# Performance work log

Measured on AMD Instinct MI355X. Metric: run time of the kernel, lower is better.

Reference implementation:

```python
import jax, jax.numpy as jnp
import numpy as np

M, A, E, H = 2048, 64, 128, 256
NUM_BOND_TYPES, NUM_ATOM_TYPES = 4, 118

def setup_inputs() -> dict:
    key = jax.random.key(0)
    ks = jax.random.split(key, 12)
    s = 0.02
    return {
        'node_rep': jax.random.normal(ks[0], (M, A, H), jnp.float32),
        'edge_index': jax.random.randint(ks[1], (M, 2, E), 0, A, jnp.int32),
        'bond_type_target': jax.random.randint(ks[2], (M, E), 0, NUM_BOND_TYPES, jnp.int32),
        'atom_type_target': jax.random.randint(ks[3], (M, A), 0, NUM_ATOM_TYPES, jnp.int32),
        'Wp1': jax.random.normal(ks[4], (H, H), jnp.float32) * s, 'bp1': jnp.zeros((H,), jnp.float32),
        'Wp2': jax.random.normal(ks[5], (H, H), jnp.float32) * s, 'bp2': jnp.zeros((H,), jnp.float32),
        'Wb1': jax.random.normal(ks[6], (2 * H, H), jnp.float32) * s, 'bb1': jnp.zeros((H,), jnp.float32),
        'Wb2': jax.random.normal(ks[7], (H, NUM_BOND_TYPES), jnp.float32) * s, 'bb2': jnp.zeros((NUM_BOND_TYPES,), jnp.float32),
        'Wa1': jax.random.normal(ks[8], (H, H), jnp.float32) * s, 'ba1': jnp.zeros((H,), jnp.float32),
        'Wa2': jax.random.normal(ks[9], (H, NUM_ATOM_TYPES), jnp.float32) * s, 'ba2': jnp.zeros((NUM_ATOM_TYPES,), jnp.float32),
    }

def _mlp(x, W1, b1, W2, b2):
    return jnp.maximum(x @ W1 + b1, 0.0) @ W2 + b2

def reference(node_rep, edge_index, bond_type_target, atom_type_target,
              Wp1, bp1, Wp2, bp2, Wb1, bb1, Wb2, bb2, Wa1, ba1, Wa2, ba2):
    # bond_if_proj: per-atom 2-layer MLP (dropout=0 -> identity)  [M,A,H]
    proj = _mlp(node_rep, Wp1, bp1, Wp2, bp2)
    # gather bond endpoint reps: index_select over atoms per molecule  [M,E,H]
    start = jnp.take_along_axis(proj, edge_index[:, 0, :, None], axis=1)
    end = jnp.take_along_axis(proj, edge_index[:, 1, :, None], axis=1)
    bt_in = jnp.concatenate([start, end], axis=-1)            # [M,E,2H]
    bt_logits = _mlp(bt_in, Wb1, bb1, Wb2, bb2)               # [M,E,4]
    bt_logp = jax.nn.log_softmax(bt_logits, axis=-1)
    # per-molecule mean CE averaged over molecules == global mean (equal sizes)
    bond_type_loss = -jnp.mean(jnp.take_along_axis(bt_logp, bond_type_target[..., None], axis=-1))
    bond_type_acc = jnp.mean((jnp.argmax(bt_logits, axis=-1) == bond_type_target).astype(jnp.float32))
    # atom type classifier on raw node reps  [M,A,118]
    at_logits = _mlp(node_rep, Wa1, ba1, Wa2, ba2)
    at_logp = jax.nn.log_softmax(at_logits, axis=-1)
    atom_type_loss = -jnp.mean(jnp.take_along_axis(at_logp, atom_type_target[..., None], axis=-1))
    atom_type_acc = jnp.mean((jnp.argmax(at_logits, axis=-1) == atom_type_target).astype(jnp.float32))
    loss = 0.5 * bond_type_loss + 0.5 * atom_type_loss
    return loss, bond_type_acc, atom_type_acc
```

## Files before the change

kernel.cpp:

```cpp
#include <hip/hip_runtime.h>
#include <hip/hip_bf16.h>

typedef __bf16 bf16x8 __attribute__((ext_vector_type(8)));
typedef float f32x16 __attribute__((ext_vector_type(16)));

__device__ inline unsigned short f2bf(float f) {
  __hip_bfloat16 h = __float2bfloat16(f);
  return *reinterpret_cast<unsigned short*>(&h);
}
__device__ inline unsigned pack2bf(float a, float b) {
  return (unsigned)f2bf(a) | ((unsigned)f2bf(b) << 16);
}
__device__ inline uint2 pack4bf(float a, float b, float c, float d) {
  uint2 r; r.x = pack2bf(a, b); r.y = pack2bf(c, d); return r;
}
__device__ inline bf16x8 as_bf16x8(uint4 v) { return __builtin_bit_cast(bf16x8, v); }
__device__ inline float bitf(unsigned u) { return __builtin_bit_cast(float, u); }
__device__ inline f32x16 mfma16(bf16x8 a, bf16x8 b, f32x16 c) {
  return __builtin_amdgcn_mfma_f32_32x32x16_bf16(a, b, c, 0, 0, 0);
}

#define BROW(XB, KK)                                                           \
  ((XB) + ((((rw + l31) << 9) + ((KK) << 5) + (h << 4)) ^ swz))

#define GEMM8(XB, W1PTR, W2PTR)                                                \
  {                                                                            \
    const unsigned char* w1_ = (const unsigned char*)(W1PTR) +                 \
                               ((cw + l31) << 5) + (h << 4);                   \
    const unsigned char* w2_ = (const unsigned char*)(W2PTR) +                 \
                               ((cw + l31) << 5) + (h << 4);                   \
    u0 = zero; u1 = zero; v0 = zero; v1 = zero;                                \
    bf16x8 pB = *(const bf16x8*)BROW(XB, 0);                                   \
    uint4 pA0 = *(const uint4*)(w1_);                                          \
    uint4 pA1 = *(const uint4*)(w1_ + 1024);                                   \
    uint4 pC0 = *(const uint4*)(w2_);                                          \
    uint4 pC1 = *(const uint4*)(w2_ + 1024);                                   \
    _Pragma("clang loop unroll(disable)")                                      \
    for (int kk = 0; kk < 16; kk += 2) {                                       \
      bf16x8 qB = *(const bf16x8*)BROW(XB, kk + 1);                            \
      uint4 qA0 = *(const uint4*)(w1_ + ((kk + 1) << 13));                     \
      uint4 qA1 = *(const uint4*)(w1_ + ((kk + 1) << 13) + 1024);              \
      uint4 qC0 = *(const uint4*)(w2_ + ((kk + 1) << 13));                     \
      uint4 qC1 = *(const uint4*)(w2_ + ((kk + 1) << 13) + 1024);              \
      u0 = mfma16(as_bf16x8(pA0), pB, u0);                                     \
      u1 = mfma16(as_bf16x8(pA1), pB, u1);                                     \
      v0 = mfma16(as_bf16x8(pC0), pB, v0);                                     \
      v1 = mfma16(as_bf16x8(pC1), pB, v1);                                     \
      if (kk + 2 < 16) {                                                       \
        pB = *(const bf16x8*)BROW(XB, kk + 2);                                 \
        pA0 = *(const uint4*)(w1_ + ((kk + 2) << 13));                         \
        pA1 = *(const uint4*)(w1_ + ((kk + 2) << 13) + 1024);                  \
        pC0 = *(const uint4*)(w2_ + ((kk + 2) << 13));                         \
        pC1 = *(const uint4*)(w2_ + ((kk + 2) << 13) + 1024);                  \
      }                                                                        \
      u0 = mfma16(as_bf16x8(qA0), qB, u0);                                     \
      u1 = mfma16(as_bf16x8(qA1), qB, u1);                                     \
      v0 = mfma16(as_bf16x8(qC0), qB, v0);                                     \
      v1 = mfma16(as_bf16x8(qC1), qB, v1);                                     \
    }                                                                          \
  }

#define WB8(DB, ACC, C, BIASPTR)                                               \
  _Pragma("unroll")                                                            \
  for (int g = 0; g < 4; ++g) {                                                \
    int xr_ = rw + l31;                                                        \
    int col = cw + (C) * 32 + g * 8 + h * 4;                                   \
    float4 bb = *(const float4*)((BIASPTR) + col);                             \
    float v0_ = fmaxf(ACC[4 * g + 0] + bb.x, 0.f);                             \
    float v1_ = fmaxf(ACC[4 * g + 1] + bb.y, 0.f);                             \
    float v2_ = fmaxf(ACC[4 * g + 2] + bb.z, 0.f);                             \
    float v3_ = fmaxf(ACC[4 * g + 3] + bb.w, 0.f);                             \
    int off = ((xr_ << 9) + (col << 1)) ^ ((xr_ & 7) << 4);                    \
    *(uint2*)((DB) + off) = pack4bf(v0_, v1_, v2_, v3_);                       \
  }

#define WB8R(DB, ACC, C)                                                       \
  _Pragma("unroll")                                                            \
  for (int g = 0; g < 4; ++g) {                                                \
    int xr_ = rw + l31;                                                        \
    int col = cw + (C) * 32 + g * 8 + h * 4;                                   \
    int off = ((xr_ << 9) + (col << 1)) ^ ((xr_ & 7) << 4);                    \
    *(uint2*)((DB) + off) = pack4bf(ACC[4 * g + 0], ACC[4 * g + 1],            \
                                    ACC[4 * g + 2], ACC[4 * g + 3]);           \
  }

#define STAGE_X(DST, SRC)                                                      \
  _Pragma("unroll")                                                            \
  for (int it = 0; it < 4; ++it) {                                             \
    int lb = (it * 1024 + tid) * 16;                                           \
    int d_ = lb ^ (((lb >> 9) & 7) << 4);                                      \
    const float4* s4 = (const float4*)((SRC) + (lb >> 1));                     \
    float4 f0 = s4[0], f1 = s4[1];                                             \
    uint4 v_ = { pack2bf(f0.x, f0.y), pack2bf(f0.z, f0.w),                     \
                 pack2bf(f1.x, f1.y), pack2bf(f1.z, f1.w) };                   \
    *(uint4*)((DST) + d_) = v_;                                                \
  }

__global__ __launch_bounds__(256) void k_pack(
    const float* __restrict__ wp1, const float* __restrict__ wa1,
    const float* __restrict__ wa2,
    unsigned short* __restrict__ dp1, unsigned short* __restrict__ da1,
    unsigned short* __restrict__ da2, float* __restrict__ accum)
{
  int b = blockIdx.x, tid = threadIdx.x;
  if (b == 0 && tid < 8) accum[tid] = 0.f;
  const float* src; unsigned short* dst; int e, logN, Nreal;
  if (b < 256)       { src = wp1; dst = dp1; e = b * 256 + tid;          logN = 8; Nreal = 256; }
  else if (b < 512)  { src = wa1; dst = da1; e = (b - 256) * 256 + tid;  logN = 8; Nreal = 256; }
  else               { src = wa2; dst = da2; e = (b - 512) * 256 + tid;  logN = 7; Nreal = 118; }
  int dk = e & 15;
  int rest = e >> 4;
  int n = rest & ((1 << logN) - 1);
  int kk = rest >> logN;
  int k = kk * 16 + dk;
  float v = (n < Nreal) ? src[k * Nreal + n] : 0.f;
  dst[e] = f2bf(v);
}

__global__ __launch_bounds__(256) void k_fold(
    const float* __restrict__ wp2, const float* __restrict__ wb1,
    const float* __restrict__ bp2, const float* __restrict__ bb1,
    unsigned short* __restrict__ dct, unsigned short* __restrict__ dcb,
    float* __restrict__ bias_e)
{
  int b = blockIdx.x, n = threadIdx.x;
  if (b < 512) {
    int k = b & 255;
    int off = (b < 256) ? 0 : 256;
    float s = 0.f;
    for (int t = 0; t < 256; ++t)
      s += wp2[k * 256 + t] * wb1[(t + off) * 256 + n];
    unsigned short* dst = (b < 256) ? dct : dcb;
    dst[((k >> 4) * 256 + n) * 16 + (k & 15)] = f2bf(s);
  } else {
    float s = bb1[n];
    for (int t = 0; t < 256; ++t)
      s += bp2[t] * (wb1[t * 256 + n] + wb1[(256 + t) * 256 + n]);
    bias_e[n] = s;
  }
}

__global__ __launch_bounds__(1024, 4) void k_mol(
    const float* __restrict__ node, const int* __restrict__ eidx,
    const int* __restrict__ btt, const int* __restrict__ att,
    const unsigned short* __restrict__ wp1p, const float* __restrict__ bp1,
    const unsigned short* __restrict__ wctp, const unsigned short* __restrict__ wcbp,
    const float* __restrict__ bias_e, const float* __restrict__ wb2,
    const float* __restrict__ bb2,
    const unsigned short* __restrict__ wa1p, const float* __restrict__ ba1,
    const unsigned short* __restrict__ wa2p, const float* __restrict__ ba2,
    float* __restrict__ accum)
{
  __shared__ __align__(16) unsigned char bufA[65536];
  __shared__ __align__(16) unsigned char bufB[65536];
  __shared__ float s_bias[256];
  __shared__ float4 s_wb2[256];
  __shared__ float s_b2a[128];
  __shared__ float s_red[32];
  const int tid = threadIdx.x;
  const int lane = tid & 63;
  const int w = tid >> 6;
  const int l31 = lane & 31;
  const int h = lane >> 5;
  const int swz = (l31 & 7) << 4;
  const int rw = (w >> 2) * 32;
  const int cw = (w & 3) * 64;
  const int m = blockIdx.x;

  STAGE_X(bufA, node + (long)m * 32768);
  if (tid < 256) {
    s_bias[tid] = bias_e[tid];
    s_wb2[tid] = ((const float4*)wb2)[tid];
  }
  if (tid < 128) s_b2a[tid] = (tid < 118) ? ba2[tid] : 0.f;
  const int t_at = att[m * 128 + (tid >> 3)];
  __syncthreads();

  f32x16 zero = {};
  f32x16 u0, u1, v0, v1;

  GEMM8(bufA, wa1p, wp1p);
  WB8(bufB, u0, 0, ba1);
  WB8(bufB, u1, 1, ba1);
  __syncthreads();
  WB8(bufA, v0, 0, bp1);
  WB8(bufA, v1, 1, bp1);
  __syncthreads();

  f32x16 aL = zero;
  {
    const int cw2 = (w & 3) * 32;
    const unsigned char* wb_ = (const unsigned char*)wa2p +
                               ((cw2 + l31) << 5) + (h << 4);
    bf16x8 pB = *(const bf16x8*)BROW(bufB, 0);
    uint4 pA = *(const uint4*)(wb_);
    _Pragma("clang loop unroll(disable)")
    for (int kk = 0; kk < 16; kk += 2) {
      bf16x8 qB = *(const bf16x8*)BROW(bufB, kk + 1);
      uint4 qA = *(const uint4*)(wb_ + ((kk + 1) << 12));
      aL = mfma16(as_bf16x8(pA), pB, aL);
      if (kk + 2 < 16) {
        pB = *(const bf16x8*)BROW(bufB, kk + 2);
        pA = *(const uint4*)(wb_ + ((kk + 2) << 12));
      }
      aL = mfma16(as_bf16x8(qA), qB, aL);
    }
  }
  __syncthreads();

  {
    const int cw2 = (w & 3) * 32;
    const int r0 = rw + l31;
    const int rx = (r0 & 7) << 4;
    #pragma unroll
    for (int g = 0; g < 4; ++g) {
      int colb = cw2 + 8 * g + 4 * h;
      uint4 val;
      val.x = __builtin_bit_cast(unsigned, aL[4 * g + 0] + s_b2a[colb + 0]);
      val.y = __builtin_bit_cast(unsigned, aL[4 * g + 1] + s_b2a[colb + 1]);
      val.z = __builtin_bit_cast(unsigned, aL[4 * g + 2] + s_b2a[colb + 2]);
      val.w = __builtin_bit_cast(unsigned, aL[4 * g + 3] + s_b2a[colb + 3]);
      *(uint4*)(bufB + (((r0 << 9) + (colb << 2)) ^ rx)) = val;
    }
  }
  __syncthreads();

  {
    const int row = tid >> 3, g8 = tid & 7;
    const unsigned char* lr = bufB + (row << 9);
    const int rx = (row & 7) << 4;
    float mx = -3.0e38f; int am = 127;
    #pragma unroll
    for (int j = 0; j < 4; ++j) {
      int ch = g8 + 8 * j;
      if (ch < 30) {
        float4 f = *(const float4*)(lr + (((ch << 4)) ^ rx));
        int c = ch * 4;
        if (f.x > mx) { mx = f.x; am = c; }
        if (f.y > mx) { mx = f.y; am = c + 1; }
        if (c + 2 < 118 && f.z > mx) { mx = f.z; am = c + 2; }
        if (c + 3 < 118 && f.w > mx) { mx = f.w; am = c + 3; }
      }
    }
    #pragma unroll
    for (int d = 1; d < 8; d <<= 1) {
      float mo = __shfl_xor(mx, d); int amo = __shfl_xor(am, d);
      if (mo > mx || (mo == mx && amo < am)) { mx = mo; am = amo; }
    }
    float s = 0.f, vt = 0.f;
    #pragma unroll
    for (int j = 0; j < 4; ++j) {
      int ch = g8 + 8 * j;
      if (ch < 30) {
        float4 f = *(const float4*)(lr + (((ch << 4)) ^ rx));
        int c = ch * 4;
        s += __expf(f.x - mx);
        s += __expf(f.y - mx);
        if (c + 2 < 118) s += __expf(f.z - mx);
        if (c + 3 < 118) s += __expf(f.w - mx);
        if (c == t_at) vt = f.x;
        if (c + 1 == t_at) vt = f.y;
        if (c + 2 == t_at) vt = f.z;
        if (c + 3 == t_at) vt = f.w;
      }
    }
    #pragma unroll
    for (int d = 1; d < 8; d <<= 1) { s += __shfl_xor(s, d); vt += __shfl_xor(vt, d); }
    float ce = 0.f, cc = 0.f;
    if (g8 == 0) { ce = __logf(s) + mx - vt; cc = (am == t_at) ? 1.f : 0.f; }
    #pragma unroll
    for (int d = 1; d < 64; d <<= 1) { ce += __shfl_xor(ce, d); cc += __shfl_xor(cc, d); }
    if (lane == 0) { s_red[w * 2] = ce; s_red[w * 2 + 1] = cc; }
  }

  GEMM8(bufA, wctp, wcbp);
  const int e_ = tid >> 2;
  const int gmol = e_ >> 7;
  const int ee = e_ & 127;
  const int es = gmol * 64 + eidx[(2 * m + gmol) * 256 + ee];
  const int ed = gmol * 64 + eidx[(2 * m + gmol) * 256 + 128 + ee];
  const int etg = btt[(2 * m + gmol) * 128 + ee];
  const float b20 = bb2[0], b21 = bb2[1], b22 = bb2[2], b23 = bb2[3];
  __syncthreads();
  if (tid == 0) {
    float sa = 0.f, sb = 0.f;
    #pragma unroll
    for (int i = 0; i < 16; ++i) { sa += s_red[2 * i]; sb += s_red[2 * i + 1]; }
    atomicAdd(accum + 2, sa);
    atomicAdd(accum + 3, sb);
  }
  WB8R(bufA, u0, 0);
  WB8R(bufA, u1, 1);
  WB8R(bufB, v0, 0);
  WB8R(bufB, v1, 1);
  __syncthreads();

  {
    const int qf = tid & 3;
    float lg0 = 0.f, lg1 = 0.f, lg2 = 0.f, lg3 = 0.f;
    #pragma unroll
    for (int j = 0; j < 8; ++j) {
      int c0 = qf * 64 + j * 8;
      int offS = ((es << 9) + (c0 << 1)) ^ ((es & 7) << 4);
      int offD = ((ed << 9) + (c0 << 1)) ^ ((ed & 7) << 4);
      uint4 us = *(const uint4*)(bufA + offS);
      uint4 ud = *(const uint4*)(bufB + offD);
      const unsigned* pu = (const unsigned*)&us;
      const unsigned* pv = (const unsigned*)&ud;
      #pragma unroll
      for (int q = 0; q < 4; ++q) {
        unsigned ua = pu[q], ub = pv[q];
        int c = c0 + 2 * q;
        float hlo = bitf(ua << 16) + bitf(ub << 16) + s_bias[c];
        float hhi = bitf(ua & 0xffff0000u) + bitf(ub & 0xffff0000u) + s_bias[c + 1];
        hlo = fmaxf(hlo, 0.f); hhi = fmaxf(hhi, 0.f);
        float4 w0 = s_wb2[c], w1 = s_wb2[c + 1];
        lg0 = fmaf(hlo, w0.x, fmaf(hhi, w1.x, lg0));
        lg1 = fmaf(hlo, w0.y, fmaf(hhi, w1.y, lg1));
        lg2 = fmaf(hlo, w0.z, fmaf(hhi, w1.z, lg2));
        lg3 = fmaf(hlo, w0.w, fmaf(hhi, w1.w, lg3));
      }
    }
    lg0 += __shfl_xor(lg0, 1); lg1 += __shfl_xor(lg1, 1);
    lg2 += __shfl_xor(lg2, 1); lg3 += __shfl_xor(lg3, 1);
    lg0 += __shfl_xor(lg0, 2); lg1 += __shfl_xor(lg1, 2);
    lg2 += __shfl_xor(lg2, 2); lg3 += __shfl_xor(lg3, 2);
    float ce = 0.f, cc = 0.f;
    if (qf == 0) {
      float l0 = lg0 + b20, l1 = lg1 + b21, l2 = lg2 + b22, l3 = lg3 + b23;
      int t = etg;
      int am = 0; float mx = l0;
      if (l1 > mx) { mx = l1; am = 1; }
      if (l2 > mx) { mx = l2; am = 2; }
      if (l3 > mx) { mx = l3; am = 3; }
      float s = __expf(l0 - mx) + __expf(l1 - mx) + __expf(l2 - mx) + __expf(l3 - mx);
      float lt = (t == 0) ? l0 : (t == 1) ? l1 : (t == 2) ? l2 : l3;
      ce = __logf(s) + mx - lt;
      cc = (am == t) ? 1.f : 0.f;
    }
    #pragma unroll
    for (int d = 1; d < 64; d <<= 1) { ce += __shfl_xor(ce, d); cc += __shfl_xor(cc, d); }
    if (lane == 0) { s_red[w * 2] = ce; s_red[w * 2 + 1] = cc; }
    __syncthreads();
    if (tid == 0) {
      float sa = 0.f, sb = 0.f;
      #pragma unroll
      for (int i = 0; i < 16; ++i) { sa += s_red[2 * i]; sb += s_red[2 * i + 1]; }
      atomicAdd(accum + 0, sa);
      atomicAdd(accum + 1, sb);
    }
  }
}

__global__ __launch_bounds__(64) void k_final(const float* __restrict__ accum,
                                              float* __restrict__ out)
{
  if (threadIdx.x == 0) {
    float bce = accum[0] / 262144.f;
    float bcc = accum[1] / 262144.f;
    float ace = accum[2] / 131072.f;
    float acc_ = accum[3] / 131072.f;
    out[0] = 0.5f * bce + 0.5f * ace;
    out[1] = bcc;
    out[2] = acc_;
  }
}

extern "C" void kernel_launch(void* const* d_in, const int* in_sizes, int n_in,
                              void* d_out, int out_size, void* d_ws, size_t ws_size,
                              hipStream_t stream)
{
  const float* node = (const float*)d_in[0];
  const int* eidx   = (const int*)d_in[1];
  const int* btt    = (const int*)d_in[2];
  const int* att    = (const int*)d_in[3];
  const float* Wp1 = (const float*)d_in[4];
  const float* bp1 = (const float*)d_in[5];
  const float* Wp2 = (const float*)d_in[6];
  const float* bp2 = (const float*)d_in[7];
  const float* Wb1 = (const float*)d_in[8];
  const float* bb1 = (const float*)d_in[9];
  const float* Wb2 = (const float*)d_in[10];
  const float* bb2 = (const float*)d_in[11];
  const float* Wa1 = (const float*)d_in[12];
  const float* ba1 = (const float*)d_in[13];
  const float* Wa2 = (const float*)d_in[14];
  const float* ba2 = (const float*)d_in[15];

  char* ws = (char*)d_ws;
  float* accum = (float*)ws;
  unsigned short* dp1 = (unsigned short*)(ws + 256);
  unsigned short* da1 = (unsigned short*)(ws + 131328);
  unsigned short* da2 = (unsigned short*)(ws + 262400);
  unsigned short* dct = (unsigned short*)(ws + 327936);
  unsigned short* dcb = (unsigned short*)(ws + 459008);
  float* bias_e       = (float*)(ws + 590080);

  k_pack<<<640, 256, 0, stream>>>(Wp1, Wa1, Wa2, dp1, da1, da2, accum);
  k_fold<<<513, 256, 0, stream>>>(Wp2, Wb1, bp2, bb1, dct, dcb, bias_e);
  k_mol<<<1024, 1024, 0, stream>>>(node, eidx, btt, att, dp1, bp1, dct, dcb,
                                   bias_e, Wb2, bb2, da1, ba1, da2, ba2, accum);
  k_final<<<1, 64, 0, stream>>>(accum, (float*)d_out);
}
```

Measured before the change: 197.1 us.

## Process one molecule per 512-thread block with 2x2 register-tiled MFMA per wave

```diff
diff --git a/kernel.cpp b/kernel.cpp
--- a/kernel.cpp
+++ b/kernel.cpp
@@ -20,50 +20,45 @@
   return __builtin_amdgcn_mfma_f32_32x32x16_bf16(a, b, c, 0, 0, 0);
 }
 
-#define BROW(XB, KK)                                                           \
-  ((XB) + ((((rw + l31) << 9) + ((KK) << 5) + (h << 4)) ^ swz))
-
-#define GEMM8(XB, W1PTR, W2PTR)                                                \
+#define BR(XB, R, KK)                                                          \
+  ((XB) + (((((R) * 32 + l31) << 9) + ((KK) << 5) + (h << 4)) ^ swz))
+
+#define GEMMS(XB, WPTR)                                                        \
   {                                                                            \
-    const unsigned char* w1_ = (const unsigned char*)(W1PTR) +                 \
+    const unsigned char* wb_ = (const unsigned char*)(WPTR) +                  \
                                ((cw + l31) << 5) + (h << 4);                   \
-    const unsigned char* w2_ = (const unsigned char*)(W2PTR) +                 \
-                               ((cw + l31) << 5) + (h << 4);                   \
-    u0 = zero; u1 = zero; v0 = zero; v1 = zero;                                \
-    bf16x8 pB = *(const bf16x8*)BROW(XB, 0);                                   \
-    uint4 pA0 = *(const uint4*)(w1_);                                          \
-    uint4 pA1 = *(const uint4*)(w1_ + 1024);                                   \
-    uint4 pC0 = *(const uint4*)(w2_);                                          \
-    uint4 pC1 = *(const uint4*)(w2_ + 1024);                                   \
+    acc00 = zero; acc01 = zero; acc10 = zero; acc11 = zero;                    \
+    bf16x8 pB0 = *(const bf16x8*)BR(XB, 0, 0);                                 \
+    bf16x8 pB1 = *(const bf16x8*)BR(XB, 1, 0);                                 \
+    uint4 pA0 = *(const uint4*)(wb_);                                          \
+    uint4 pA1 = *(const uint4*)(wb_ + 1024);                                   \
     _Pragma("clang loop unroll(disable)")                                      \
     for (int kk = 0; kk < 16; kk += 2) {                                       \
-      bf16x8 qB = *(const bf16x8*)BROW(XB, kk + 1);                            \
-      uint4 qA0 = *(const uint4*)(w1_ + ((kk + 1) << 13));                     \
-      uint4 qA1 = *(const uint4*)(w1_ + ((kk + 1) << 13) + 1024);              \
-      uint4 qC0 = *(const uint4*)(w2_ + ((kk + 1) << 13));                     \
-      uint4 qC1 = *(const uint4*)(w2_ + ((kk + 1) << 13) + 1024);              \
-      u0 = mfma16(as_bf16x8(pA0), pB, u0);                                     \
-      u1 = mfma16(as_bf16x8(pA1), pB, u1);                                     \
-      v0 = mfma16(as_bf16x8(pC0), pB, v0);                                     \
-      v1 = mfma16(as_bf16x8(pC1), pB, v1);                                     \
+      bf16x8 qB0 = *(const bf16x8*)BR(XB, 0, kk + 1);                          \
+      bf16x8 qB1 = *(const bf16x8*)BR(XB, 1, kk + 1);                          \
+      uint4 qA0 = *(const uint4*)(wb_ + ((kk + 1) << 13));                     \
+      uint4 qA1 = *(const uint4*)(wb_ + ((kk + 1) << 13) + 1024);              \
+      acc00 = mfma16(as_bf16x8(pA0), pB0, acc00);                              \
+      acc10 = mfma16(as_bf16x8(pA1), pB0, acc10);                              \
+      acc01 = mfma16(as_bf16x8(pA0), pB1, acc01);                              \
+      acc11 = mfma16(as_bf16x8(pA1), pB1, acc11);                              \
       if (kk + 2 < 16) {                                                       \
-        pB = *(const bf16x8*)BROW(XB, kk + 2);                                 \
-        pA0 = *(const uint4*)(w1_ + ((kk + 2) << 13));                         \
-        pA1 = *(const uint4*)(w1_ + ((kk + 2) << 13) + 1024);                  \
-        pC0 = *(const uint4*)(w2_ + ((kk + 2) << 13));                         \
-        pC1 = *(const uint4*)(w2_ + ((kk + 2) << 13) + 1024);                  \
+        pB0 = *(const bf16x8*)BR(XB, 0, kk + 2);                               \
+        pB1 = *(const bf16x8*)BR(XB, 1, kk + 2);                               \
+        pA0 = *(const uint4*)(wb_ + ((kk + 2) << 13));                         \
+        pA1 = *(const uint4*)(wb_ + ((kk + 2) << 13) + 1024);                  \
       }                                                                        \
-      u0 = mfma16(as_bf16x8(qA0), qB, u0);                                     \
-      u1 = mfma16(as_bf16x8(qA1), qB, u1);                                     \
-      v0 = mfma16(as_bf16x8(qC0), qB, v0);                                     \
-      v1 = mfma16(as_bf16x8(qC1), qB, v1);                                     \
+      acc00 = mfma16(as_bf16x8(qA0), qB0, acc00);                              \
+      acc10 = mfma16(as_bf16x8(qA1), qB0, acc10);                              \
+      acc01 = mfma16(as_bf16x8(qA0), qB1, acc01);                              \
+      acc11 = mfma16(as_bf16x8(qA1), qB1, acc11);                              \
     }                                                                          \
   }
 
-#define WB8(DB, ACC, C, BIASPTR)                                               \
+#define WB22(DB, ACC, R, C, BIASPTR)                                           \
   _Pragma("unroll")                                                            \
   for (int g = 0; g < 4; ++g) {                                                \
-    int xr_ = rw + l31;                                                        \
+    int xr_ = (R) * 32 + l31;                                                  \
     int col = cw + (C) * 32 + g * 8 + h * 4;                                   \
     float4 bb = *(const float4*)((BIASPTR) + col);                             \
     float v0_ = fmaxf(ACC[4 * g + 0] + bb.x, 0.f);                             \
@@ -74,10 +69,10 @@
     *(uint2*)((DB) + off) = pack4bf(v0_, v1_, v2_, v3_);                       \
   }
 
-#define WB8R(DB, ACC, C)                                                       \
+#define WB22R(DB, ACC, R, C)                                                   \
   _Pragma("unroll")                                                            \
   for (int g = 0; g < 4; ++g) {                                                \
-    int xr_ = rw + l31;                                                        \
+    int xr_ = (R) * 32 + l31;                                                  \
     int col = cw + (C) * 32 + g * 8 + h * 4;                                   \
     int off = ((xr_ << 9) + (col << 1)) ^ ((xr_ & 7) << 4);                    \
     *(uint2*)((DB) + off) = pack4bf(ACC[4 * g + 0], ACC[4 * g + 1],            \
@@ -87,7 +82,7 @@
 #define STAGE_X(DST, SRC)                                                      \
   _Pragma("unroll")                                                            \
   for (int it = 0; it < 4; ++it) {                                             \
-    int lb = (it * 1024 + tid) * 16;                                           \
+    int lb = (it * 512 + tid) * 16;                                            \
     int d_ = lb ^ (((lb >> 9) & 7) << 4);                                      \
     const float4* s4 = (const float4*)((SRC) + (lb >> 1));                     \
     float4 f0 = s4[0], f1 = s4[1];                                             \
@@ -140,7 +135,7 @@
   }
 }
 
-__global__ __launch_bounds__(1024, 4) void k_mol(
+__global__ __launch_bounds__(512, 4) void k_mol(
     const float* __restrict__ node, const int* __restrict__ eidx,
     const int* __restrict__ btt, const int* __restrict__ att,
     const unsigned short* __restrict__ wp1p, const float* __restrict__ bp1,
@@ -151,56 +146,65 @@
     const unsigned short* __restrict__ wa2p, const float* __restrict__ ba2,
     float* __restrict__ accum)
 {
-  __shared__ __align__(16) unsigned char bufA[65536];
-  __shared__ __align__(16) unsigned char bufB[65536];
+  __shared__ __align__(16) unsigned char bufA[32768];
+  __shared__ __align__(16) unsigned char bufB[32768];
   __shared__ float s_bias[256];
   __shared__ float4 s_wb2[256];
   __shared__ float s_b2a[128];
-  __shared__ float s_red[32];
+  __shared__ float s_red[16];
   const int tid = threadIdx.x;
   const int lane = tid & 63;
   const int w = tid >> 6;
   const int l31 = lane & 31;
   const int h = lane >> 5;
   const int swz = (l31 & 7) << 4;
-  const int rw = (w >> 2) * 32;
+  const int mat = w >> 2;
   const int cw = (w & 3) * 64;
   const int m = blockIdx.x;
 
-  STAGE_X(bufA, node + (long)m * 32768);
+  STAGE_X(bufA, node + (long)m * 16384);
   if (tid < 256) {
     s_bias[tid] = bias_e[tid];
     s_wb2[tid] = ((const float4*)wb2)[tid];
   }
   if (tid < 128) s_b2a[tid] = (tid < 118) ? ba2[tid] : 0.f;
-  const int t_at = att[m * 128 + (tid >> 3)];
+  const int t_at = att[m * 64 + (tid >> 3)];
   __syncthreads();
 
   f32x16 zero = {};
-  f32x16 u0, u1, v0, v1;
-
-  GEMM8(bufA, wa1p, wp1p);
-  WB8(bufB, u0, 0, ba1);
-  WB8(bufB, u1, 1, ba1);
-  __syncthreads();
-  WB8(bufA, v0, 0, bp1);
-  WB8(bufA, v1, 1, bp1);
+  f32x16 acc00, acc01, acc10, acc11;
+
+  GEMMS(bufA, mat ? wp1p : wa1p);
+  if (mat == 0) {
+    WB22(bufB, acc00, 0, 0, ba1);
+    WB22(bufB, acc10, 0, 1, ba1);
+    WB22(bufB, acc01, 1, 0, ba1);
+    WB22(bufB, acc11, 1, 1, ba1);
+  }
+  __syncthreads();
+  if (mat == 1) {
+    WB22(bufA, acc00, 0, 0, bp1);
+    WB22(bufA, acc10, 0, 1, bp1);
+    WB22(bufA, acc01, 1, 0, bp1);
+    WB22(bufA, acc11, 1, 1, bp1);
+  }
   __syncthreads();
 
   f32x16 aL = zero;
   {
     const int cw2 = (w & 3) * 32;
+    const int R2 = w >> 2;
     const unsigned char* wb_ = (const unsigned char*)wa2p +
                                ((cw2 + l31) << 5) + (h << 4);
-    bf16x8 pB = *(const bf16x8*)BROW(bufB, 0);
+    bf16x8 pB = *(const bf16x8*)BR(bufB, R2, 0);
     uint4 pA = *(const uint4*)(wb_);
     _Pragma("clang loop unroll(disable)")
     for (int kk = 0; kk < 16; kk += 2) {
-      bf16x8 qB = *(const bf16x8*)BROW(bufB, kk + 1);
+      bf16x8 qB = *(const bf16x8*)BR(bufB, R2, kk + 1);
       uint4 qA = *(const uint4*)(wb_ + ((kk + 1) << 12));
       aL = mfma16(as_bf16x8(pA), pB, aL);
       if (kk + 2 < 16) {
-        pB = *(const bf16x8*)BROW(bufB, kk + 2);
+        pB = *(const bf16x8*)BR(bufB, R2, kk + 2);
         pA = *(const uint4*)(wb_ + ((kk + 2) << 12));
       }
       aL = mfma16(as_bf16x8(qA), qB, aL);
@@ -210,7 +214,7 @@
 
   {
     const int cw2 = (w & 3) * 32;
-    const int r0 = rw + l31;
+    const int r0 = (w >> 2) * 32 + l31;
     const int rx = (r0 & 7) << 4;
     #pragma unroll
     for (int g = 0; g < 4; ++g) {
@@ -273,26 +277,30 @@
     if (lane == 0) { s_red[w * 2] = ce; s_red[w * 2 + 1] = cc; }
   }
 
-  GEMM8(bufA, wctp, wcbp);
-  const int e_ = tid >> 2;
-  const int gmol = e_ >> 7;
-  const int ee = e_ & 127;
-  const int es = gmol * 64 + eidx[(2 * m + gmol) * 256 + ee];
-  const int ed = gmol * 64 + eidx[(2 * m + gmol) * 256 + 128 + ee];
-  const int etg = btt[(2 * m + gmol) * 128 + ee];
+  GEMMS(bufA, mat ? wcbp : wctp);
+  const int es = eidx[m * 256 + (tid >> 2)];
+  const int ed = eidx[m * 256 + 128 + (tid >> 2)];
+  const int etg = btt[m * 128 + (tid >> 2)];
   const float b20 = bb2[0], b21 = bb2[1], b22 = bb2[2], b23 = bb2[3];
   __syncthreads();
   if (tid == 0) {
     float sa = 0.f, sb = 0.f;
     #pragma unroll
-    for (int i = 0; i < 16; ++i) { sa += s_red[2 * i]; sb += s_red[2 * i + 1]; }
+    for (int i = 0; i < 8; ++i) { sa += s_red[2 * i]; sb += s_red[2 * i + 1]; }
     atomicAdd(accum + 2, sa);
     atomicAdd(accum + 3, sb);
   }
-  WB8R(bufA, u0, 0);
-  WB8R(bufA, u1, 1);
-  WB8R(bufB, v0, 0);
-  WB8R(bufB, v1, 1);
+  if (mat == 0) {
+    WB22R(bufA, acc00, 0, 0);
+    WB22R(bufA, acc10, 0, 1);
+    WB22R(bufA, acc01, 1, 0);
+    WB22R(bufA, acc11, 1, 1);
+  } else {
+    WB22R(bufB, acc00, 0, 0);
+    WB22R(bufB, acc10, 0, 1);
+    WB22R(bufB, acc01, 1, 0);
+    WB22R(bufB, acc11, 1, 1);
+  }
   __syncthreads();
 
   {
@@ -345,7 +353,7 @@
     if (tid == 0) {
       float sa = 0.f, sb = 0.f;
       #pragma unroll
-      for (int i = 0; i < 16; ++i) { sa += s_red[2 * i]; sb += s_red[2 * i + 1]; }
+      for (int i = 0; i < 8; ++i) { sa += s_red[2 * i]; sb += s_red[2 * i + 1]; }
       atomicAdd(accum + 0, sa);
       atomicAdd(accum + 1, sb);
     }
@@ -398,7 +406,7 @@
 
   k_pack<<<640, 256, 0, stream>>>(Wp1, Wa1, Wa2, dp1, da1, da2, accum);
   k_fold<<<513, 256, 0, stream>>>(Wp2, Wb1, bp2, bb1, dct, dcb, bias_e);
-  k_mol<<<1024, 1024, 0, stream>>>(node, eidx, btt, att, dp1, bp1, dct, dcb,
-                                   bias_e, Wb2, bb2, da1, ba1, da2, ba2, accum);
+  k_mol<<<2048, 512, 0, stream>>>(node, eidx, btt, att, dp1, bp1, dct, dcb,
+                                  bias_e, Wb2, bb2, da1, ba1, da2, ba2, accum);
   k_final<<<1, 64, 0, stream>>>(accum, (float*)d_out);
 }
```

Result: no change. 200.0 us (+1.5%).

## Process one molecule per block and fuse the bond GEMM with the atom logits GEMM

Applied to the files above, without the earlier changes.

```diff
diff --git a/kernel.cpp b/kernel.cpp
--- a/kernel.cpp
+++ b/kernel.cpp
@@ -42,10 +42,12 @@
       uint4 qA1 = *(const uint4*)(w1_ + ((kk + 1) << 13) + 1024);              \
       uint4 qC0 = *(const uint4*)(w2_ + ((kk + 1) << 13));                     \
       uint4 qC1 = *(const uint4*)(w2_ + ((kk + 1) << 13) + 1024);              \
+      __builtin_amdgcn_s_setprio(1);                                           \
       u0 = mfma16(as_bf16x8(pA0), pB, u0);                                     \
       u1 = mfma16(as_bf16x8(pA1), pB, u1);                                     \
       v0 = mfma16(as_bf16x8(pC0), pB, v0);                                     \
       v1 = mfma16(as_bf16x8(pC1), pB, v1);                                     \
+      __builtin_amdgcn_s_setprio(0);                                           \
       if (kk + 2 < 16) {                                                       \
         pB = *(const bf16x8*)BROW(XB, kk + 2);                                 \
         pA0 = *(const uint4*)(w1_ + ((kk + 2) << 13));                         \
@@ -53,10 +55,12 @@
         pC0 = *(const uint4*)(w2_ + ((kk + 2) << 13));                         \
         pC1 = *(const uint4*)(w2_ + ((kk + 2) << 13) + 1024);                  \
       }                                                                        \
+      __builtin_amdgcn_s_setprio(1);                                           \
       u0 = mfma16(as_bf16x8(qA0), qB, u0);                                     \
       u1 = mfma16(as_bf16x8(qA1), qB, u1);                                     \
       v0 = mfma16(as_bf16x8(qC0), qB, v0);                                     \
       v1 = mfma16(as_bf16x8(qC1), qB, v1);                                     \
+      __builtin_amdgcn_s_setprio(0);                                           \
     }                                                                          \
   }
 
@@ -87,7 +91,7 @@
 #define STAGE_X(DST, SRC)                                                      \
   _Pragma("unroll")                                                            \
   for (int it = 0; it < 4; ++it) {                                             \
-    int lb = (it * 1024 + tid) * 16;                                           \
+    int lb = (it * 512 + tid) * 16;                                            \
     int d_ = lb ^ (((lb >> 9) & 7) << 4);                                      \
     const float4* s4 = (const float4*)((SRC) + (lb >> 1));                     \
     float4 f0 = s4[0], f1 = s4[1];                                             \
@@ -107,7 +111,7 @@
   const float* src; unsigned short* dst; int e, logN, Nreal;
   if (b < 256)       { src = wp1; dst = dp1; e = b * 256 + tid;          logN = 8; Nreal = 256; }
   else if (b < 512)  { src = wa1; dst = da1; e = (b - 256) * 256 + tid;  logN = 8; Nreal = 256; }
-  else               { src = wa2; dst = da2; e = (b - 512) * 256 + tid;  logN = 7; Nreal = 118; }
+  else               { src = wa2; dst = da2; e = (b - 512) * 256 + tid; logN = 7; Nreal = 118; }
   int dk = e & 15;
   int rest = e >> 4;
   int n = rest & ((1 << logN) - 1);
@@ -140,7 +144,7 @@
   }
 }
 
-__global__ __launch_bounds__(1024, 4) void k_mol(
+__global__ __launch_bounds__(512, 4) void k_mol(
     const float* __restrict__ node, const int* __restrict__ eidx,
     const int* __restrict__ btt, const int* __restrict__ att,
     const unsigned short* __restrict__ wp1p, const float* __restrict__ bp1,
@@ -151,12 +155,12 @@
     const unsigned short* __restrict__ wa2p, const float* __restrict__ ba2,
     float* __restrict__ accum)
 {
-  __shared__ __align__(16) unsigned char bufA[65536];
-  __shared__ __align__(16) unsigned char bufB[65536];
+  __shared__ __align__(16) unsigned char bufA[32768];
+  __shared__ __align__(16) unsigned char bufB[32768];
   __shared__ float s_bias[256];
   __shared__ float4 s_wb2[256];
   __shared__ float s_b2a[128];
-  __shared__ float s_red[32];
+  __shared__ float s_red[16];
   const int tid = threadIdx.x;
   const int lane = tid & 63;
   const int w = tid >> 6;
@@ -167,13 +171,13 @@
   const int cw = (w & 3) * 64;
   const int m = blockIdx.x;
 
-  STAGE_X(bufA, node + (long)m * 32768);
+  STAGE_X(bufA, node + (long)m * 16384);
   if (tid < 256) {
     s_bias[tid] = bias_e[tid];
     s_wb2[tid] = ((const float4*)wb2)[tid];
   }
   if (tid < 128) s_b2a[tid] = (tid < 118) ? ba2[tid] : 0.f;
-  const int t_at = att[m * 128 + (tid >> 3)];
+  const int t_at = att[m * 64 + (tid >> 3)];
   __syncthreads();
 
   f32x16 zero = {};
@@ -187,29 +191,64 @@
   WB8(bufA, v1, 1, bp1);
   __syncthreads();
 
+  const int cw2 = (w & 3) * 32;
   f32x16 aL = zero;
   {
-    const int cw2 = (w & 3) * 32;
-    const unsigned char* wb_ = (const unsigned char*)wa2p +
+    const unsigned char* w1_ = (const unsigned char*)wctp +
+                               ((cw + l31) << 5) + (h << 4);
+    const unsigned char* w2_ = (const unsigned char*)wcbp +
+                               ((cw + l31) << 5) + (h << 4);
+    const unsigned char* w3_ = (const unsigned char*)wa2p +
                                ((cw2 + l31) << 5) + (h << 4);
-    bf16x8 pB = *(const bf16x8*)BROW(bufB, 0);
-    uint4 pA = *(const uint4*)(wb_);
+    u0 = zero; u1 = zero; v0 = zero; v1 = zero;
+    bf16x8 pB  = *(const bf16x8*)BROW(bufA, 0);
+    bf16x8 pBL = *(const bf16x8*)BROW(bufB, 0);
+    uint4 pA0 = *(const uint4*)(w1_);
+    uint4 pA1 = *(const uint4*)(w1_ + 1024);
+    uint4 pC0 = *(const uint4*)(w2_);
+    uint4 pC1 = *(const uint4*)(w2_ + 1024);
+    uint4 pL  = *(const uint4*)(w3_);
     _Pragma("clang loop unroll(disable)")
     for (int kk = 0; kk < 16; kk += 2) {
-      bf16x8 qB = *(const bf16x8*)BROW(bufB, kk + 1);
-      uint4 qA = *(const uint4*)(wb_ + ((kk + 1) << 12));
-      aL = mfma16(as_bf16x8(pA), pB, aL);
+      bf16x8 qB  = *(const bf16x8*)BROW(bufA, kk + 1);
+      bf16x8 qBL = *(const bf16x8*)BROW(bufB, kk + 1);
+      uint4 qA0 = *(const uint4*)(w1_ + ((kk + 1) << 13));
+      uint4 qA1 = *(const uint4*)(w1_ + ((kk + 1) << 13) + 1024);
+      uint4 qC0 = *(const uint4*)(w2_ + ((kk + 1) << 13));
+      uint4 qC1 = *(const uint4*)(w2_ + ((kk + 1) << 13) + 1024);
+      uint4 qL  = *(const uint4*)(w3_ + ((kk + 1) << 12));
+      __builtin_amdgcn_s_setprio(1);
+      u0 = mfma16(as_bf16x8(pA0), pB, u0);
+      u1 = mfma16(as_bf16x8(pA1), pB, u1);
+      v0 = mfma16(as_bf16x8(pC0), pB, v0);
+      v1 = mfma16(as_bf16x8(pC1), pB, v1);
+      aL = mfma16(as_bf16x8(pL), pBL, aL);
+      __builtin_amdgcn_s_setprio(0);
       if (kk + 2 < 16) {
-        pB = *(const bf16x8*)BROW(bufB, kk + 2);
-        pA = *(const uint4*)(wb_ + ((kk + 2) << 12));
+        pB  = *(const bf16x8*)BROW(bufA, kk + 2);
+        pBL = *(const bf16x8*)BROW(bufB, kk + 2);
+        pA0 = *(const uint4*)(w1_ + ((kk + 2) << 13));
+        pA1 = *(const uint4*)(w1_ + ((kk + 2) << 13) + 1024);
+        pC0 = *(const uint4*)(w2_ + ((kk + 2) << 13));
+        pC1 = *(const uint4*)(w2_ + ((kk + 2) << 13) + 1024);
+        pL  = *(const uint4*)(w3_ + ((kk + 2) << 12));
       }
-      aL = mfma16(as_bf16x8(qA), qB, aL);
-    }
-  }
+      __builtin_amdgcn_s_setprio(1);
+      u0 = mfma16(as_bf16x8(qA0), qB, u0);
+      u1 = mfma16(as_bf16x8(qA1), qB, u1);
+      v0 = mfma16(as_bf16x8(qC0), qB, v0);
+      v1 = mfma16(as_bf16x8(qC1), qB, v1);
+      aL = mfma16(as_bf16x8(qL), qBL, aL);
+      __builtin_amdgcn_s_setprio(0);
+    }
+  }
+  const int es = eidx[m * 256 + (tid >> 2)];
+  const int ed = eidx[m * 256 + 128 + (tid >> 2)];
+  const int etg = btt[m * 128 + (tid >> 2)];
+  const float b20 = bb2[0], b21 = bb2[1], b22 = bb2[2], b23 = bb2[3];
   __syncthreads();
 
   {
-    const int cw2 = (w & 3) * 32;
     const int r0 = rw + l31;
     const int rx = (r0 & 7) << 4;
     #pragma unroll
@@ -223,6 +262,8 @@
       *(uint4*)(bufB + (((r0 << 9) + (colb << 2)) ^ rx)) = val;
     }
   }
+  WB8R(bufA, u0, 0);
+  WB8R(bufA, u1, 1);
   __syncthreads();
 
   {
@@ -272,25 +313,14 @@
     for (int d = 1; d < 64; d <<= 1) { ce += __shfl_xor(ce, d); cc += __shfl_xor(cc, d); }
     if (lane == 0) { s_red[w * 2] = ce; s_red[w * 2 + 1] = cc; }
   }
-
-  GEMM8(bufA, wctp, wcbp);
-  const int e_ = tid >> 2;
-  const int gmol = e_ >> 7;
-  const int ee = e_ & 127;
-  const int es = gmol * 64 + eidx[(2 * m + gmol) * 256 + ee];
-  const int ed = gmol * 64 + eidx[(2 * m + gmol) * 256 + 128 + ee];
-  const int etg = btt[(2 * m + gmol) * 128 + ee];
-  const float b20 = bb2[0], b21 = bb2[1], b22 = bb2[2], b23 = bb2[3];
   __syncthreads();
   if (tid == 0) {
     float sa = 0.f, sb = 0.f;
     #pragma unroll
-    for (int i = 0; i < 16; ++i) { sa += s_red[2 * i]; sb += s_red[2 * i + 1]; }
+    for (int i = 0; i < 8; ++i) { sa += s_red[2 * i]; sb += s_red[2 * i + 1]; }
     atomicAdd(accum + 2, sa);
     atomicAdd(accum + 3, sb);
   }
-  WB8R(bufA, u0, 0);
-  WB8R(bufA, u1, 1);
   WB8R(bufB, v0, 0);
   WB8R(bufB, v1, 1);
   __syncthreads();
@@ -345,7 +375,7 @@
     if (tid == 0) {
       float sa = 0.f, sb = 0.f;
       #pragma unroll
-      for (int i = 0; i < 16; ++i) { sa += s_red[2 * i]; sb += s_red[2 * i + 1]; }
+      for (int i = 0; i < 8; ++i) { sa += s_red[2 * i]; sb += s_red[2 * i + 1]; }
       atomicAdd(accum + 0, sa);
       atomicAdd(accum + 1, sb);
     }
@@ -398,7 +428,7 @@
 
   k_pack<<<640, 256, 0, stream>>>(Wp1, Wa1, Wa2, dp1, da1, da2, accum);
   k_fold<<<513, 256, 0, stream>>>(Wp2, Wb1, bp2, bb1, dct, dcb, bias_e);
-  k_mol<<<1024, 1024, 0, stream>>>(node, eidx, btt, att, dp1, bp1, dct, dcb,
-                                   bias_e, Wb2, bb2, da1, ba1, da2, ba2, accum);
+  k_mol<<<2048, 512, 0, stream>>>(node, eidx, btt, att, dp1, bp1, dct, dcb,
+                                  bias_e, Wb2, bb2, da1, ba1, da2, ba2, accum);
   k_final<<<1, 64, 0, stream>>>(accum, (float*)d_out);
 }
```

Result: slower. 423.8 us (+115.0%).
